# Kernel tuning notes

Measured on AMD Instinct MI355X. Metric: run time of the kernel, lower is better.

The kernel has to match this reference:

```python
import jax, jax.numpy as jnp
import numpy as np

B, T, D, H, C = 256, 512, 128, 512, 10

def setup_inputs() -> dict:
    key = jax.random.key(0)
    ks = jax.random.split(key, 16)
    def kn(k, shape):  # kaiming-normal-ish init (gain irrelevant for correctness)
        fan_in = shape[-1]
        return jax.random.normal(k, shape, dtype=jnp.float32) * (1.0 / np.sqrt(fan_in))
    return {
        "x": jax.random.randint(ks[0], (B, T), 0, 3),
        "emb": jax.random.normal(ks[1], (3, D), dtype=jnp.float32),
        "Wfx": kn(ks[2], (H, D)), "Wfh": kn(ks[3], (H, H)), "bf": jnp.zeros((H,), jnp.float32),
        "Wix": kn(ks[4], (H, D)), "Wih": kn(ks[5], (H, H)), "bi": jnp.zeros((H,), jnp.float32),
        "Wox": kn(ks[6], (H, D)), "Woh": kn(ks[7], (H, H)), "bo": jnp.zeros((H,), jnp.float32),
        "Wcx": kn(ks[8], (H, D)), "bc": jnp.zeros((H,), jnp.float32),
        "Wph": kn(ks[9], (C, H)), "bp": jnp.zeros((C,), jnp.float32),
    }

def _forward(x, emb, Wfx, Wfh, bf, Wix, Wih, bi, Wox, Woh, bo, Wcx, bc, Wph, bp):
    xe = emb[x]  # [B, T, D]
    # Precompute input-to-gate projections as one big batched matmul each.
    fx = jnp.einsum('btd,hd->bth', xe, Wfx) + bf  # [B, T, H]
    ix = jnp.einsum('btd,hd->bth', xe, Wix) + bi
    ox = jnp.einsum('btd,hd->bth', xe, Wox) + bo
    cx = jnp.einsum('btd,hd->bth', xe, Wcx) + bc
    gates = jnp.stack([fx, ix, ox, cx], axis=0).transpose(2, 1, 0, 3)  # [T, B, 4, H]

    def step(carry, g):
        c, _ = carry
        gf, gi, go, gc = g[:, 0], g[:, 1], g[:, 2], g[:, 3]  # each [B, H]
        f = jax.nn.sigmoid(gf + c @ Wfh.T)
        i = jax.nn.sigmoid(gi + c @ Wih.T)
        o = jax.nn.sigmoid(go + c @ Woh.T)
        c_new = jax.nn.sigmoid(gc) * i + c * f
        h = jnp.tanh(c_new) * o
        return (c_new, h), None

    c0 = jnp.zeros((x.shape[0], Wfh.shape[0]), jnp.float32)
    (c_fin, h_fin), _ = jax.lax.scan(step, (c0, c0), gates)
    p = h_fin @ Wph.T + bp
    return jax.nn.log_softmax(p, axis=1)

def reference(x, emb, Wfx, Wfh, bf, Wix, Wih, bi, Wox, Woh, bo, Wcx, bc, Wph, bp):
    return _forward(x, emb, Wfx, Wfh, bf, Wix, Wih, bi, Wox, Woh, bo, Wcx, bc, Wph, bp)
```

## Files before the change

### kernel.cpp

```cpp
#include <hip/hip_runtime.h>
#include <stdint.h>

#define TLEN 512
#define HDIM 512
#define DDIM 128
#define NCLS 10

typedef float f32x4 __attribute__((ext_vector_type(4)));
typedef short bf16x8 __attribute__((ext_vector_type(8)));

__device__ __forceinline__ unsigned short f2bf(float f) {
  union { float f; unsigned u; } v; v.f = f;
  return (unsigned short)((v.u + 0x7FFFu + ((v.u >> 16) & 1u)) >> 16);
}
__device__ __forceinline__ float bf2f(unsigned short h) {
  union { unsigned u; float f; } v; v.u = ((unsigned)h) << 16; return v.f;
}
__device__ __forceinline__ float sigm(float x) {
  return __builtin_amdgcn_rcpf(1.0f + __expf(-x));
}

__global__ void k_init(int* __restrict__ cnt) {
  if (threadIdx.x < 16) cnt[threadIdx.x] = 0;
}

__global__ void k_gates(const float* __restrict__ emb,
                        const float* __restrict__ Wfx, const float* __restrict__ bf_,
                        const float* __restrict__ Wix, const float* __restrict__ bi_,
                        const float* __restrict__ Wcx, const float* __restrict__ bc_,
                        const float* __restrict__ Wox, const float* __restrict__ bo_,
                        float* __restrict__ G) {
  int tid = blockIdx.x * 256 + threadIdx.x;
  int h = tid & (HDIM - 1);
  int v = (tid >> 9) % 3;
  int g = tid / (3 * HDIM);
  const float* W; const float* bb;
  if (g == 0)      { W = Wfx; bb = bf_; }
  else if (g == 1) { W = Wix; bb = bi_; }
  else if (g == 2) { W = Wcx; bb = bc_; }
  else             { W = Wox; bb = bo_; }
  const float* e = emb + v * DDIM;
  const float* w = W + h * DDIM;
  float s = bb[h];
  #pragma unroll 8
  for (int d = 0; d < DDIM; ++d) s += e[d] * w[d];
  if (g == 2) s = sigm(s);
  G[tid] = s;
}

__global__ void k_pack_fi(const float* __restrict__ Wfh, const float* __restrict__ Wih,
                          unsigned short* __restrict__ pk) {
  int tid = blockIdx.x * 256 + threadIdx.x;
  int l  = tid & 63;
  int kt = (tid >> 6) & 15;
  int g  = (tid >> 10) & 1;
  int nt = (tid >> 11) & 3;
  int hs = (tid >> 13) & 7;
  int n  = hs * 64 + nt * 16 + (l & 15);
  int k0 = kt * 32 + (l >> 4) * 8;
  const float* src = (g ? Wih : Wfh) + n * HDIM + k0;
  unsigned short* dst = pk + (size_t)tid * 8;
  #pragma unroll
  for (int e = 0; e < 8; ++e) dst[e] = f2bf(src[e]);
}

__global__ void k_pack_o(const float* __restrict__ Woh, unsigned short* __restrict__ pk) {
  int tid = blockIdx.x * 256 + threadIdx.x;
  int l  = tid & 63;
  int kt = (tid >> 6) & 15;
  int nt = (tid >> 10) & 3;
  int hs = (tid >> 12) & 7;
  int n  = hs * 64 + nt * 16 + (l & 15);
  int k0 = kt * 32 + (l >> 4) * 8;
  const float* src = Woh + n * HDIM + k0;
  unsigned short* dst = pk + (size_t)tid * 8;
  #pragma unroll
  for (int e = 0; e < 8; ++e) dst[e] = f2bf(src[e]);
}

__global__ __launch_bounds__(256, 1)
void k_scan(const int* __restrict__ x, const float* __restrict__ G,
            const unsigned short* __restrict__ pk2,
            const unsigned short* __restrict__ pko,
            unsigned int* __restrict__ cbuf, int* __restrict__ cnt,
            unsigned short* __restrict__ hfin) {
  __shared__ float gts[12][68];
  __shared__ unsigned char xv[16][516];
  __shared__ unsigned short ctile[16][66];

  const int tid  = threadIdx.x;
  const int lane = tid & 63;
  const int w    = tid >> 6;
  const int bt   = blockIdx.x & 15;
  const int hs   = blockIdx.x >> 4;

  for (int j = tid; j < 12 * 64; j += 256) {
    int gv = j >> 6, c = j & 63;
    gts[gv][c] = G[gv * HDIM + hs * 64 + c];
  }
  for (int j = tid; j < 16 * TLEN; j += 256) {
    int r = j >> 9, t = j & (TLEN - 1);
    xv[r][t] = (unsigned char)x[(bt * 16 + r) * TLEN + t];
  }

  bf16x8 wf[16], wi[16];
  {
    const bf16x8* ws = (const bf16x8*)pk2 + (size_t)((hs * 4 + w) * 2) * (16 * 64) + lane;
    #pragma unroll
    for (int kt = 0; kt < 16; ++kt) { wf[kt] = ws[kt * 64]; wi[kt] = ws[(16 + kt) * 64]; }
  }

  bf16x8 afr[16];
  #pragma unroll
  for (int kt = 0; kt < 16; ++kt) afr[kt] = bf16x8{0,0,0,0,0,0,0,0};

  float cf[4] = {0.f, 0.f, 0.f, 0.f};
  const int rgrp = (lane >> 4) * 4;
  const int coll = lane & 15;
  const int col  = w * 16 + coll;
  const f32x4 zz = {0.f, 0.f, 0.f, 0.f};
  int* mycnt = cnt + bt;

  __syncthreads();

  for (int t = 0; t < TLEN - 1; ++t) {
    f32x4 af = zz, ai = zz;
    #pragma unroll
    for (int kt = 0; kt < 16; ++kt) {
      af = __builtin_amdgcn_mfma_f32_16x16x32_bf16(afr[kt], wf[kt], af, 0, 0, 0);
      ai = __builtin_amdgcn_mfma_f32_16x16x32_bf16(afr[kt], wi[kt], ai, 0, 0, 0);
    }
    #pragma unroll
    for (int r = 0; r < 4; ++r) {
      int vv = xv[rgrp + r][t];
      float fg = sigm(af[r] + gts[0 + vv][col]);
      float ig = sigm(ai[r] + gts[3 + vv][col]);
      float sc = gts[6 + vv][col];
      float cn = sc * ig + cf[r] * fg;
      cf[r] = cn;
      ctile[rgrp + r][col] = f2bf(cn);
    }
    __syncthreads();

    const unsigned bufo = (unsigned)((((t + 1) & 1) * 16 + bt) * 4096);
    #pragma unroll
    for (int h2 = 0; h2 < 2; ++h2) {
      int d   = tid + h2 * 256;
      int ktl = d >> 8, rem = d & 255, lp = rem >> 2, ep = rem & 3;
      int m   = lp & 15;
      int cl  = ktl * 32 + (lp >> 4) * 8 + ep * 2;
      unsigned val = *(const unsigned*)&ctile[m][cl];
      __hip_atomic_store(cbuf + bufo + (unsigned)((hs * 2 + ktl) * 256 + lp * 4 + ep),
                         val, __ATOMIC_RELAXED, __HIP_MEMORY_SCOPE_AGENT);
    }
    __syncthreads();

    if (tid == 0)
      __hip_atomic_fetch_add(mycnt, 1, __ATOMIC_RELAXED, __HIP_MEMORY_SCOPE_AGENT);
    const int target = 8 * (t + 1);
    while (__hip_atomic_load(mycnt, __ATOMIC_RELAXED, __HIP_MEMORY_SCOPE_AGENT) < target)
      __builtin_amdgcn_s_sleep(1);
    asm volatile("" ::: "memory");

    const unsigned long long* ap = (const unsigned long long*)(cbuf + bufo) + (size_t)lane * 2;
    #pragma unroll
    for (int kt = 0; kt < 16; ++kt) {
      unsigned long long lo = __hip_atomic_load(ap + (size_t)kt * 128 + 0,
                                                __ATOMIC_RELAXED, __HIP_MEMORY_SCOPE_AGENT);
      unsigned long long hi = __hip_atomic_load(ap + (size_t)kt * 128 + 1,
                                                __ATOMIC_RELAXED, __HIP_MEMORY_SCOPE_AGENT);
      union { unsigned long long q[2]; bf16x8 v; } u;
      u.q[0] = lo; u.q[1] = hi;
      afr[kt] = u.v;
    }
  }

  {
    const int t = TLEN - 1;
    bf16x8 wo[16];
    const bf16x8* os = (const bf16x8*)pko + (size_t)(hs * 4 + w) * (16 * 64) + lane;
    #pragma unroll
    for (int kt = 0; kt < 16; ++kt) wo[kt] = os[kt * 64];
    f32x4 af = zz, ai = zz, ao = zz;
    #pragma unroll
    for (int kt = 0; kt < 16; ++kt) {
      af = __builtin_amdgcn_mfma_f32_16x16x32_bf16(afr[kt], wf[kt], af, 0, 0, 0);
      ai = __builtin_amdgcn_mfma_f32_16x16x32_bf16(afr[kt], wi[kt], ai, 0, 0, 0);
      ao = __builtin_amdgcn_mfma_f32_16x16x32_bf16(afr[kt], wo[kt], ao, 0, 0, 0);
    }
    #pragma unroll
    for (int r = 0; r < 4; ++r) {
      int vv = xv[rgrp + r][t];
      float fg = sigm(af[r] + gts[0 + vv][col]);
      float ig = sigm(ai[r] + gts[3 + vv][col]);
      float sc = gts[6 + vv][col];
      float cn = sc * ig + cf[r] * fg;
      float og = sigm(ao[r] + gts[9 + vv][col]);
      float hv = tanhf(cn) * og;
      hfin[(bt * 16 + rgrp + r) * HDIM + hs * 64 + col] = f2bf(hv);
    }
  }
}

__global__ __launch_bounds__(64)
void k_head(const unsigned short* __restrict__ hfin, const float* __restrict__ Wph,
            const float* __restrict__ bp, float* __restrict__ out) {
  const int b = blockIdx.x;
  const int lane = threadIdx.x;
  float acc[NCLS];
  #pragma unroll
  for (int c = 0; c < NCLS; ++c) acc[c] = 0.f;
  const unsigned short* hrow = hfin + (size_t)b * HDIM;
  for (int k = lane; k < HDIM; k += 64) {
    float hv = bf2f(hrow[k]);
    #pragma unroll
    for (int c = 0; c < NCLS; ++c) acc[c] += hv * Wph[c * HDIM + k];
  }
  #pragma unroll
  for (int c = 0; c < NCLS; ++c)
    #pragma unroll
    for (int off = 32; off > 0; off >>= 1)
      acc[c] += __shfl_down(acc[c], off, 64);
  if (lane == 0) {
    float p[NCLS]; float m = -1e30f;
    #pragma unroll
    for (int c = 0; c < NCLS; ++c) { p[c] = acc[c] + bp[c]; m = fmaxf(m, p[c]); }
    float s = 0.f;
    #pragma unroll
    for (int c = 0; c < NCLS; ++c) s += __expf(p[c] - m);
    const float ls = __logf(s);
    #pragma unroll
    for (int c = 0; c < NCLS; ++c) out[b * NCLS + c] = p[c] - m - ls;
  }
}

extern "C" void kernel_launch(void* const* d_in, const int* in_sizes, int n_in,
                              void* d_out, int out_size, void* d_ws, size_t ws_size,
                              hipStream_t stream) {
  const int*   x   = (const int*)d_in[0];
  const float* emb = (const float*)d_in[1];
  const float* Wfx = (const float*)d_in[2];
  const float* Wfh = (const float*)d_in[3];
  const float* bf_ = (const float*)d_in[4];
  const float* Wix = (const float*)d_in[5];
  const float* Wih = (const float*)d_in[6];
  const float* bi_ = (const float*)d_in[7];
  const float* Wox = (const float*)d_in[8];
  const float* Woh = (const float*)d_in[9];
  const float* bo_ = (const float*)d_in[10];
  const float* Wcx = (const float*)d_in[11];
  const float* bc_ = (const float*)d_in[12];
  const float* Wph = (const float*)d_in[13];
  const float* bp_ = (const float*)d_in[14];

  char* ws = (char*)d_ws;
  float*          G    = (float*)(ws);
  int*            cnt  = (int*)(ws + 24576);
  unsigned short* hfin = (unsigned short*)(ws + 32768);
  unsigned int*   cbuf = (unsigned int*)(ws + 524288);
  unsigned short* pk2  = (unsigned short*)(ws + 1048576);
  unsigned short* pko  = (unsigned short*)(ws + 2097152);

  hipLaunchKernelGGL(k_init,    dim3(1),   dim3(64),  0, stream, cnt);
  hipLaunchKernelGGL(k_gates,   dim3(24),  dim3(256), 0, stream,
                     emb, Wfx, bf_, Wix, bi_, Wcx, bc_, Wox, bo_, G);
  hipLaunchKernelGGL(k_pack_fi, dim3(256), dim3(256), 0, stream, Wfh, Wih, pk2);
  hipLaunchKernelGGL(k_pack_o,  dim3(128), dim3(256), 0, stream, Woh, pko);
  hipLaunchKernelGGL(k_scan,    dim3(128), dim3(256), 0, stream, x, G, pk2, pko, cbuf, cnt, hfin);
  hipLaunchKernelGGL(k_head,    dim3(256), dim3(64),  0, stream, hfin, Wph, bp_, (float*)d_out);
}
```

Baseline: 1.466 ms.

## Replace counter barrier with per-element timestamped flags in scan exchange

Each cell-state value is now written to global memory as a 32-bit word tagged with the step number. Consumers spin on those tags directly instead of waiting on a shared atomic counter after two block barriers and a staging copy. Each wave polls a quarter of the A tiles and shares them with the other waves through double-buffered LDS, which removes one __syncthreads and the serial counter round trip per timestep. The cost is double the exchange traffic (32-bit words instead of packed bf16) plus a memset of a larger buffer, and correctness now depends on tag/data atomicity within each word.

```diff
diff --git a/kernel.cpp b/kernel.cpp
--- a/kernel.cpp
+++ b/kernel.cpp
@@ -8,6 +8,7 @@
 
 typedef float f32x4 __attribute__((ext_vector_type(4)));
 typedef short bf16x8 __attribute__((ext_vector_type(8)));
+typedef unsigned long long u64;
 
 __device__ __forceinline__ unsigned short f2bf(float f) {
   union { float f; unsigned u; } v; v.f = f;
@@ -19,9 +20,11 @@
 __device__ __forceinline__ float sigm(float x) {
   return __builtin_amdgcn_rcpf(1.0f + __expf(-x));
 }
-
-__global__ void k_init(int* __restrict__ cnt) {
-  if (threadIdx.x < 16) cnt[threadIdx.x] = 0;
+__device__ __forceinline__ u64 ald(const u64* p) {
+  return __hip_atomic_load(p, __ATOMIC_RELAXED, __HIP_MEMORY_SCOPE_AGENT);
+}
+__device__ __forceinline__ void ast(unsigned* p, unsigned v) {
+  __hip_atomic_store(p, v, __ATOMIC_RELAXED, __HIP_MEMORY_SCOPE_AGENT);
 }
 
 __global__ void k_gates(const float* __restrict__ emb,
@@ -82,11 +85,11 @@
 void k_scan(const int* __restrict__ x, const float* __restrict__ G,
             const unsigned short* __restrict__ pk2,
             const unsigned short* __restrict__ pko,
-            unsigned int* __restrict__ cbuf, int* __restrict__ cnt,
+            unsigned* __restrict__ cbuf,
             unsigned short* __restrict__ hfin) {
   __shared__ float gts[12][68];
   __shared__ unsigned char xv[16][516];
-  __shared__ unsigned short ctile[16][66];
+  __shared__ uint4 lds_a[2][16][64];
 
   const int tid  = threadIdx.x;
   const int lane = tid & 63;
@@ -99,8 +102,8 @@
     gts[gv][c] = G[gv * HDIM + hs * 64 + c];
   }
   for (int j = tid; j < 16 * TLEN; j += 256) {
-    int r = j >> 9, t = j & (TLEN - 1);
-    xv[r][t] = (unsigned char)x[(bt * 16 + r) * TLEN + t];
+    int r = j >> 9, tt = j & (TLEN - 1);
+    xv[r][tt] = (unsigned char)x[(bt * 16 + r) * TLEN + tt];
   }
 
   bf16x8 wf[16], wi[16];
@@ -119,7 +122,11 @@
   const int coll = lane & 15;
   const int col  = w * 16 + coll;
   const f32x4 zz = {0.f, 0.f, 0.f, 0.f};
-  int* mycnt = cnt + bt;
+
+  u64* cb64 = (u64*)cbuf;
+  const int qoff = bt * 4096 + (lane & 15) * 256 + (lane >> 4) * 4;
+  const int poff = bt * 8192 + hs * 64 + col;
+  const u64 msk = 0xFFFF0000FFFF0000ULL;
 
   __syncthreads();
 
@@ -130,6 +137,9 @@
       af = __builtin_amdgcn_mfma_f32_16x16x32_bf16(afr[kt], wf[kt], af, 0, 0, 0);
       ai = __builtin_amdgcn_mfma_f32_16x16x32_bf16(afr[kt], wi[kt], ai, 0, 0, 0);
     }
+    const unsigned tg = (unsigned)(t + 1);
+    const int par = (t + 1) & 1;
+    const int sbase = par * 131072 + poff;
     #pragma unroll
     for (int r = 0; r < 4; ++r) {
       int vv = xv[rgrp + r][t];
@@ -138,39 +148,41 @@
       float sc = gts[6 + vv][col];
       float cn = sc * ig + cf[r] * fg;
       cf[r] = cn;
-      ctile[rgrp + r][col] = f2bf(cn);
-    }
+      ast(cbuf + sbase + (rgrp + r) * 512, (tg << 16) | (unsigned)f2bf(cn));
+    }
+    asm volatile("" ::: "memory");
+
+    const u64 pat = ((u64)tg << 48) | ((u64)tg << 16);
+    const u64* qb = cb64 + (size_t)par * 65536 + qoff;
+    u64 a[4][4];
+    #pragma unroll
+    for (int ktl = 0; ktl < 4; ++ktl) {
+      const u64* p = qb + (size_t)((w << 2) | ktl) * 16;
+      a[ktl][0] = ald(p + 0); a[ktl][1] = ald(p + 1);
+      a[ktl][2] = ald(p + 2); a[ktl][3] = ald(p + 3);
+    }
+    uint4 got[4];
+    #pragma unroll
+    for (int ktl = 0; ktl < 4; ++ktl) {
+      const u64* p = qb + (size_t)((w << 2) | ktl) * 16;
+      while ((((a[ktl][0] ^ pat) | (a[ktl][1] ^ pat) |
+               (a[ktl][2] ^ pat) | (a[ktl][3] ^ pat)) & msk) != 0ULL) {
+        a[ktl][0] = ald(p + 0); a[ktl][1] = ald(p + 1);
+        a[ktl][2] = ald(p + 2); a[ktl][3] = ald(p + 3);
+      }
+      got[ktl].x = (unsigned)(a[ktl][0] & 0xFFFF) | ((unsigned)(a[ktl][0] >> 32) << 16);
+      got[ktl].y = (unsigned)(a[ktl][1] & 0xFFFF) | ((unsigned)(a[ktl][1] >> 32) << 16);
+      got[ktl].z = (unsigned)(a[ktl][2] & 0xFFFF) | ((unsigned)(a[ktl][2] >> 32) << 16);
+      got[ktl].w = (unsigned)(a[ktl][3] & 0xFFFF) | ((unsigned)(a[ktl][3] >> 32) << 16);
+    }
+    #pragma unroll
+    for (int ktl = 0; ktl < 4; ++ktl)
+      lds_a[par][(w << 2) | ktl][lane] = got[ktl];
     __syncthreads();
-
-    const unsigned bufo = (unsigned)((((t + 1) & 1) * 16 + bt) * 4096);
-    #pragma unroll
-    for (int h2 = 0; h2 < 2; ++h2) {
-      int d   = tid + h2 * 256;
-      int ktl = d >> 8, rem = d & 255, lp = rem >> 2, ep = rem & 3;
-      int m   = lp & 15;
-      int cl  = ktl * 32 + (lp >> 4) * 8 + ep * 2;
-      unsigned val = *(const unsigned*)&ctile[m][cl];
-      __hip_atomic_store(cbuf + bufo + (unsigned)((hs * 2 + ktl) * 256 + lp * 4 + ep),
-                         val, __ATOMIC_RELAXED, __HIP_MEMORY_SCOPE_AGENT);
-    }
-    __syncthreads();
-
-    if (tid == 0)
-      __hip_atomic_fetch_add(mycnt, 1, __ATOMIC_RELAXED, __HIP_MEMORY_SCOPE_AGENT);
-    const int target = 8 * (t + 1);
-    while (__hip_atomic_load(mycnt, __ATOMIC_RELAXED, __HIP_MEMORY_SCOPE_AGENT) < target)
-      __builtin_amdgcn_s_sleep(1);
-    asm volatile("" ::: "memory");
-
-    const unsigned long long* ap = (const unsigned long long*)(cbuf + bufo) + (size_t)lane * 2;
     #pragma unroll
     for (int kt = 0; kt < 16; ++kt) {
-      unsigned long long lo = __hip_atomic_load(ap + (size_t)kt * 128 + 0,
-                                                __ATOMIC_RELAXED, __HIP_MEMORY_SCOPE_AGENT);
-      unsigned long long hi = __hip_atomic_load(ap + (size_t)kt * 128 + 1,
-                                                __ATOMIC_RELAXED, __HIP_MEMORY_SCOPE_AGENT);
-      union { unsigned long long q[2]; bf16x8 v; } u;
-      u.q[0] = lo; u.q[1] = hi;
+      union { uint4 q; bf16x8 v; } u;
+      u.q = lds_a[par][kt][lane];
       afr[kt] = u.v;
     }
   }
@@ -255,17 +267,16 @@
 
   char* ws = (char*)d_ws;
   float*          G    = (float*)(ws);
-  int*            cnt  = (int*)(ws + 24576);
   unsigned short* hfin = (unsigned short*)(ws + 32768);
-  unsigned int*   cbuf = (unsigned int*)(ws + 524288);
-  unsigned short* pk2  = (unsigned short*)(ws + 1048576);
-  unsigned short* pko  = (unsigned short*)(ws + 2097152);
-
-  hipLaunchKernelGGL(k_init,    dim3(1),   dim3(64),  0, stream, cnt);
+  unsigned*       cbuf = (unsigned*)(ws + 524288);
+  unsigned short* pk2  = (unsigned short*)(ws + 1572864);
+  unsigned short* pko  = (unsigned short*)(ws + 2621440);
+
+  hipMemsetAsync(cbuf, 0, 1048576, stream);
   hipLaunchKernelGGL(k_gates,   dim3(24),  dim3(256), 0, stream,
                      emb, Wfx, bf_, Wix, bi_, Wcx, bc_, Wox, bo_, G);
   hipLaunchKernelGGL(k_pack_fi, dim3(256), dim3(256), 0, stream, Wfh, Wih, pk2);
   hipLaunchKernelGGL(k_pack_o,  dim3(128), dim3(256), 0, stream, Woh, pko);
-  hipLaunchKernelGGL(k_scan,    dim3(128), dim3(256), 0, stream, x, G, pk2, pko, cbuf, cnt, hfin);
+  hipLaunchKernelGGL(k_scan,    dim3(128), dim3(256), 0, stream, x, G, pk2, pko, cbuf, hfin);
   hipLaunchKernelGGL(k_head,    dim3(256), dim3(64),  0, stream, hfin, Wph, bp_, (float*)d_out);
 }
```

After: 2.436 ms. 1.66x slower.
